# Performance work log

Measured on AMD Instinct MI355X. Metric: run time of the kernel, lower is better.

Reference implementation:

```python
import jax, jax.numpy as jnp
import numpy as np

D_MODEL = 1024
NUM_HEADS = 16
DEPTH = D_MODEL // NUM_HEADS
B, S = 2, 2048


def setup_inputs() -> dict:
    key = jax.random.key(0)
    ks = jax.random.split(key, 12)
    s = 1.0 / np.sqrt(D_MODEL)
    return {
        "query": jax.random.normal(ks[0], (B, S, D_MODEL), jnp.float32),
        "key": jax.random.normal(ks[1], (B, S, D_MODEL), jnp.float32),
        "value": jax.random.normal(ks[2], (B, S, D_MODEL), jnp.float32),
        "mask": jax.random.randint(ks[3], (B, S), 0, 2, jnp.int32),
        "Wq": jax.random.normal(ks[4], (D_MODEL, D_MODEL), jnp.float32) * s,
        "bq": jnp.zeros((D_MODEL,), jnp.float32),
        "Wk": jax.random.normal(ks[5], (D_MODEL, D_MODEL), jnp.float32) * s,
        "bk": jnp.zeros((D_MODEL,), jnp.float32),
        "Wv": jax.random.normal(ks[6], (D_MODEL, D_MODEL), jnp.float32) * s,
        "bv": jnp.zeros((D_MODEL,), jnp.float32),
        "Wo": jax.random.normal(ks[7], (D_MODEL, D_MODEL), jnp.float32) * s,
        "bo": jnp.zeros((D_MODEL,), jnp.float32),
    }


def _split_heads(x):
    # [B, S, D] -> [B, H, S, depth]
    b, s, _ = x.shape
    return x.reshape(b, s, NUM_HEADS, DEPTH).transpose(0, 2, 1, 3)


def reference(query, key, value, mask, Wq, bq, Wk, bk, Wv, bv, Wo, bo):
    q = _split_heads(query @ Wq.T + bq)
    k = _split_heads(key @ Wk.T + bk)
    v = _split_heads(value @ Wv.T + bv)
    scale = 1.0 / jnp.sqrt(jnp.float32(DEPTH))
    # [B, H, Sq, Sk]
    logits = jnp.einsum("bhqd,bhkd->bhqk", q, k) * scale
    logits = logits + mask.astype(logits.dtype)[:, None, None, :] * (-1e9)
    attn = jax.nn.softmax(logits, axis=-1)
    out = jnp.einsum("bhqk,bhkd->bhqd", attn, v)
    out = out.transpose(0, 2, 1, 3).reshape(query.shape[0], -1, D_MODEL)
    return out @ Wo.T + bo
```

## Files before the change

kernel.cpp:

```cpp
#include <hip/hip_runtime.h>

typedef _Float16 half8 __attribute__((ext_vector_type(8)));
typedef _Float16 half4 __attribute__((ext_vector_type(4)));
typedef __fp16  fp16x2 __attribute__((ext_vector_type(2)));
typedef float floatx4 __attribute__((ext_vector_type(4)));

#define D_MODEL 1024
#define NHEAD   16
#define DH      64
#define BATCH   2
#define SEQ     2048
#define M_TOT   4096

#define SCALE_L2E 0.18033688011112042f
#define MASK_L2E  (-1.4426950408889634e9f)

#define GLD_LDS16(g, l)                                                          \
  __builtin_amdgcn_global_load_lds(                                              \
      (const __attribute__((address_space(1))) void*)(g),                        \
      (__attribute__((address_space(3))) void*)(l), 16, 0, 0)

__device__ inline half4 pk4(floatx4 v) {
  union { fp16x2 h2[2]; half4 h4; } u;
  u.h2[0] = __builtin_amdgcn_cvt_pkrtz(v[0], v[1]);
  u.h2[1] = __builtin_amdgcn_cvt_pkrtz(v[2], v[3]);
  return u.h4;
}

__global__ __launch_bounds__(256) void cvt_all(const float* __restrict__ q,
                                               const float* __restrict__ k,
                                               const float* __restrict__ v,
                                               const float* __restrict__ wq,
                                               const float* __restrict__ wk,
                                               const float* __restrict__ wv,
                                               const float* __restrict__ wo,
                                               _Float16* __restrict__ Xall,
                                               _Float16* __restrict__ Wall) {
  int bid = blockIdx.x;
  const float* src;
  _Float16* dst;
  if (bid < 6144) {
    int tsr = bid >> 11;
    src = (tsr == 0) ? q : (tsr == 1) ? k : v;
    dst = Xall + (size_t)tsr * 4194304;
    bid &= 2047;
  } else {
    int w = (bid - 6144) >> 9;
    src = (w == 0) ? wq : (w == 1) ? wk : (w == 2) ? wv : wo;
    dst = Wall + (size_t)w * 1048576;
    bid = (bid - 6144) & 511;
  }
  int off = bid * 2048 + threadIdx.x * 8;
  float4 a = *(const float4*)(src + off);
  float4 b = *(const float4*)(src + off + 4);
  half8 h;
  h[0] = (_Float16)a.x; h[1] = (_Float16)a.y; h[2] = (_Float16)a.z; h[3] = (_Float16)a.w;
  h[4] = (_Float16)b.x; h[5] = (_Float16)b.y; h[6] = (_Float16)b.z; h[7] = (_Float16)b.w;
  *(half8*)(dst + off) = h;
}

__global__ __launch_bounds__(256) void gemm_qkv(const _Float16* __restrict__ Xall,
                                                const _Float16* __restrict__ Wall,
                                                const float* __restrict__ bq,
                                                const float* __restrict__ bk,
                                                const float* __restrict__ bv,
                                                _Float16* __restrict__ Obase) {
  __shared__ alignas(16) char smem[32768];
  _Float16 (*As)[64]  = (_Float16(*)[64])smem;
  _Float16 (*Bs)[64]  = (_Float16(*)[64])(smem + 16384);
  _Float16 (*Ts)[136] = (_Float16(*)[136])smem;

  const int z = blockIdx.z;
  const _Float16* X = Xall + (size_t)z * 4194304;
  const _Float16* W = Wall + (size_t)z * 1048576;
  const float* bias = (z == 0) ? bq : (z == 1) ? bk : bv;
  _Float16* out = Obase + (size_t)z * 4194304;

  const int t = threadIdx.x, lane = t & 63, wave = t >> 6;
  const int wr = wave >> 1, wc = wave & 1;
  const int m0 = blockIdx.y * 128, n0 = blockIdx.x * 128;
  const int fr = lane & 15, quad = lane >> 4, rg = quad * 4;
  const int fsw = fr & 7;

  floatx4 acc[4][4];
  for (int i = 0; i < 4; i++)
    for (int j = 0; j < 4; j++) acc[i][j] = (floatx4){0.f, 0.f, 0.f, 0.f};

  const int rl = lane >> 3, pc = lane & 7;
  const int gcol = ((pc ^ rl) * 8);
  const _Float16* gA[4];
  const _Float16* gB[4];
  _Float16* lA[4];
  _Float16* lB[4];
  for (int i = 0; i < 4; i++) {
    int row = wave * 32 + i * 8 + rl;
    gA[i] = X + (size_t)(m0 + row) * 1024 + gcol;
    gB[i] = W + (size_t)(n0 + row) * 1024 + gcol;
    lA[i] = &As[wave * 32 + i * 8][0];
    lB[i] = &Bs[wave * 32 + i * 8][0];
  }

  for (int k0 = 0; k0 < 1024; k0 += 64) {
    for (int i = 0; i < 4; i++) GLD_LDS16(gA[i] + k0, lA[i]);
    for (int i = 0; i < 4; i++) GLD_LDS16(gB[i] + k0, lB[i]);
    __syncthreads();

    for (int kk = 0; kk < 2; kk++) {
      const int csw = (((kk << 2) | quad) ^ fsw) * 8;
      half8 af[4], bw[4];
      for (int i = 0; i < 4; i++) {
        af[i] = *(const half8*)&As[wr * 64 + i * 16 + fr][csw];
        bw[i] = *(const half8*)&Bs[wc * 64 + i * 16 + fr][csw];
      }
      for (int i = 0; i < 4; i++)
        for (int j = 0; j < 4; j++)
          acc[i][j] = __builtin_amdgcn_mfma_f32_16x16x32_f16(af[i], bw[j], acc[i][j], 0, 0, 0);
    }
    __syncthreads();
  }

  if (z != 2) {
    for (int i = 0; i < 4; i++)
      for (int j = 0; j < 4; j++) {
        int n = n0 + wc * 64 + j * 16 + fr;
        float bv2 = bias[n];
        int hh = n >> 6, d = n & 63;
        for (int r = 0; r < 4; r++) {
          int m = m0 + wr * 64 + i * 16 + rg + r;
          int bb = m >> 11, s = m & 2047;
          out[(((size_t)(bb * NHEAD + hh)) * SEQ + s) * DH + d] =
              (_Float16)(acc[i][j][r] + bv2);
        }
      }
  } else {
    const int bb = m0 >> 11, s0 = m0 & 2047;
    for (int p = 0; p < 2; p++) {
      __syncthreads();
      if (wc == p) {
        for (int j = 0; j < 4; j++) {
          float bv2 = bias[n0 + p * 64 + j * 16 + fr];
          for (int i = 0; i < 4; i++)
            for (int r = 0; r < 4; r++)
              Ts[j * 16 + fr][wr * 64 + i * 16 + rg + r] =
                  (_Float16)(acc[i][j][r] + bv2);
        }
      }
      __syncthreads();
      int dd = t >> 2, c4 = (t & 3) * 32;
      int hh = (n0 >> 6) + p;
      _Float16* dst = out + (((size_t)(bb * NHEAD + hh)) * DH + dd) * SEQ + s0;
      for (int u = 0; u < 4; u++)
        *(half8*)(dst + c4 + u * 8) = *(const half8*)&Ts[dd][c4 + u * 8];
    }
  }
}

__global__ __launch_bounds__(256) void gemm_wo(const _Float16* __restrict__ ctx,
                                               const _Float16* __restrict__ W,
                                               const float* __restrict__ bias,
                                               float* __restrict__ out) {
  __shared__ alignas(16) _Float16 As[128][64];
  __shared__ alignas(16) _Float16 Bs[64][64];

  const int t = threadIdx.x, lane = t & 63, wave = t >> 6;
  const int m0 = blockIdx.y * 128, n0 = blockIdx.x * 64;
  const int fr = lane & 15, quad = lane >> 4, rg = quad * 4;
  const int fsw = fr & 7;

  floatx4 acc[2][4];
  for (int i = 0; i < 2; i++)
    for (int j = 0; j < 4; j++) acc[i][j] = (floatx4){0.f, 0.f, 0.f, 0.f};

  const int rl = lane >> 3, pc = lane & 7;
  const int gcol = ((pc ^ rl) * 8);
  const _Float16* gA[4];
  const _Float16* gB[2];
  _Float16* lA[4];
  _Float16* lB[2];
  for (int i = 0; i < 4; i++) {
    int row = wave * 32 + i * 8 + rl;
    gA[i] = ctx + (size_t)(m0 + row) * 1024 + gcol;
    lA[i] = &As[wave * 32 + i * 8][0];
  }
  for (int i = 0; i < 2; i++) {
    int row = wave * 16 + i * 8 + rl;
    gB[i] = W + (size_t)(n0 + row) * 1024 + gcol;
    lB[i] = &Bs[wave * 16 + i * 8][0];
  }

  for (int k0 = 0; k0 < 1024; k0 += 64) {
    for (int i = 0; i < 4; i++) GLD_LDS16(gA[i] + k0, lA[i]);
    for (int i = 0; i < 2; i++) GLD_LDS16(gB[i] + k0, lB[i]);
    __syncthreads();

    for (int kk = 0; kk < 2; kk++) {
      const int csw = (((kk << 2) | quad) ^ fsw) * 8;
      half8 af[2], bw[4];
      for (int i = 0; i < 2; i++)
        af[i] = *(const half8*)&As[wave * 32 + i * 16 + fr][csw];
      for (int j = 0; j < 4; j++)
        bw[j] = *(const half8*)&Bs[j * 16 + fr][csw];
      for (int i = 0; i < 2; i++)
        for (int j = 0; j < 4; j++)
          acc[i][j] = __builtin_amdgcn_mfma_f32_16x16x32_f16(af[i], bw[j], acc[i][j], 0, 0, 0);
    }
    __syncthreads();
  }

  for (int i = 0; i < 2; i++)
    for (int j = 0; j < 4; j++) {
      int n = n0 + j * 16 + fr;
      float bv2 = bias[n];
      for (int r = 0; r < 4; r++) {
        int m = m0 + wave * 32 + i * 16 + rg + r;
        out[(size_t)m * D_MODEL + n] = acc[i][j][r] + bv2;
      }
    }
}

__global__ __launch_bounds__(256) void attn_kernel(const _Float16* __restrict__ Qp,
                                                   const _Float16* __restrict__ Kp,
                                                   const _Float16* __restrict__ VT,
                                                   const int* __restrict__ mask,
                                                   _Float16* __restrict__ ctx) {
  __shared__ alignas(16) _Float16 Ks[128][64];
  __shared__ alignas(16) _Float16 Vt[64][128];
  __shared__ float Msf[128];

  const int b = blockIdx.z, h = blockIdx.y, q0 = blockIdx.x * 128;
  const int t = threadIdx.x, lane = t & 63, wave = t >> 6;
  const int fr = lane & 15, quad = lane >> 4, fc = quad * 8;
  const int fsw = fr & 7;

  const _Float16* Kg  = Kp + (size_t)(b * NHEAD + h) * SEQ * DH;
  const _Float16* VTg = VT + (size_t)(b * NHEAD + h) * DH * SEQ;

  half8 qf[2][2];
  {
    const _Float16* Qgw = Qp + ((size_t)(b * NHEAD + h) * SEQ + q0 + wave * 32) * DH;
    for (int mi = 0; mi < 2; mi++)
      for (int kk = 0; kk < 2; kk++)
        qf[mi][kk] = *(const half8*)(Qgw + (mi * 16 + fr) * DH + kk * 32 + fc);
  }

  float lrow[2] = {0.f, 0.f};
  floatx4 oaccT[4][2];
  for (int dj = 0; dj < 4; dj++)
    for (int mi = 0; mi < 2; mi++) oaccT[dj][mi] = (floatx4){0.f, 0.f, 0.f, 0.f};

  const int skr = t >> 1;
  const int skc = (t & 1) * 4;
  const int svr = t >> 2;
  const int svc = (t & 3) * 4;

  for (int kt = 0; kt < SEQ / 128; kt++) {
    const int k0 = kt * 128;
    {
      const half8* gk = (const half8*)(Kg + (k0 + skr) * 64);
      for (int u = 0; u < 4; u++)
        *(half8*)&Ks[skr][((skc + u) ^ (skr & 7)) * 8] = gk[skc + u];
      const half8* gv = (const half8*)(VTg + (size_t)svr * SEQ + k0);
      for (int u = 0; u < 4; u++)
        *(half8*)&Vt[svr][((svc + u) ^ (svr & 7)) * 8] = gv[svc + u];
      if (t < 128) Msf[t] = (float)mask[b * SEQ + k0 + t] * MASK_L2E;
    }
    __syncthreads();

    floatx4 saT[8][2];
#pragma unroll
    for (int t8 = 0; t8 < 8; t8++) {
      saT[t8][0] = (floatx4){0.f, 0.f, 0.f, 0.f};
      saT[t8][1] = (floatx4){0.f, 0.f, 0.f, 0.f};
      half8 kf0 = *(const half8*)&Ks[t8 * 16 + fr][(quad ^ fsw) * 8];
      half8 kf1 = *(const half8*)&Ks[t8 * 16 + fr][((4 | quad) ^ fsw) * 8];
      saT[t8][0] = __builtin_amdgcn_mfma_f32_16x16x32_f16(kf0, qf[0][0], saT[t8][0], 0, 0, 0);
      saT[t8][1] = __builtin_amdgcn_mfma_f32_16x16x32_f16(kf0, qf[1][0], saT[t8][1], 0, 0, 0);
      saT[t8][0] = __builtin_amdgcn_mfma_f32_16x16x32_f16(kf1, qf[0][1], saT[t8][0], 0, 0, 0);
      saT[t8][1] = __builtin_amdgcn_mfma_f32_16x16x32_f16(kf1, qf[1][1], saT[t8][1], 0, 0, 0);
    }

    floatx4 mk[8];
#pragma unroll
    for (int t8 = 0; t8 < 8; t8++)
      mk[t8] = *(const floatx4*)&Msf[t8 * 16 + quad * 4];

#pragma unroll
    for (int mi = 0; mi < 2; mi++) {
      float rs = 0.f;
#pragma unroll
      for (int t8 = 0; t8 < 8; t8++)
        for (int r = 0; r < 4; r++) {
          float p = exp2f(saT[t8][mi][r] * SCALE_L2E + mk[t8][r]);
          saT[t8][mi][r] = p;
          rs += p;
        }
      lrow[mi] += rs;
    }

#pragma unroll
    for (int t8 = 0; t8 < 8; t8++) {
      half4 pb0 = pk4(saT[t8][0]);
      half4 pb1 = pk4(saT[t8][1]);
      const int ch0 = t8 * 2 + (quad >> 1);
      const int voff = ((ch0 ^ fsw) * 8) + (quad & 1) * 4;
#pragma unroll
      for (int dj = 0; dj < 4; dj++) {
        half4 va = *(const half4*)&Vt[dj * 16 + fr][voff];
        oaccT[dj][0] = __builtin_amdgcn_mfma_f32_16x16x16f16(va, pb0, oaccT[dj][0], 0, 0, 0);
        oaccT[dj][1] = __builtin_amdgcn_mfma_f32_16x16x16f16(va, pb1, oaccT[dj][1], 0, 0, 0);
      }
    }
    __syncthreads();
  }

#pragma unroll
  for (int mi = 0; mi < 2; mi++) {
    float l = lrow[mi];
    l += __shfl_xor(l, 16);
    l += __shfl_xor(l, 32);
    float inv = 1.0f / l;
    int qrow = q0 + wave * 32 + mi * 16 + fr;
    _Float16* o = ctx + ((size_t)b * SEQ + qrow) * D_MODEL + h * DH;
#pragma unroll
    for (int dj = 0; dj < 4; dj++) {
      half4 st;
      for (int r = 0; r < 4; r++) st[r] = (_Float16)(oaccT[dj][mi][r] * inv);
      *(half4*)(o + dj * 16 + quad * 4) = st;
    }
  }
}

extern "C" void kernel_launch(void* const* d_in, const int* in_sizes, int n_in,
                              void* d_out, int out_size, void* d_ws, size_t ws_size,
                              hipStream_t stream) {
  const float* query = (const float*)d_in[0];
  const float* key   = (const float*)d_in[1];
  const float* value = (const float*)d_in[2];
  const int*   mask  = (const int*)d_in[3];
  const float* Wq = (const float*)d_in[4];
  const float* bq = (const float*)d_in[5];
  const float* Wk = (const float*)d_in[6];
  const float* bk = (const float*)d_in[7];
  const float* Wv = (const float*)d_in[8];
  const float* bv = (const float*)d_in[9];
  const float* Wo = (const float*)d_in[10];
  const float* bo = (const float*)d_in[11];

  char* ws = (char*)d_ws;
  _Float16* Xall = (_Float16*)(ws);
  _Float16* Wall = (_Float16*)(ws + (size_t)24 * 1024 * 1024);
  _Float16* Qp   = (_Float16*)(ws + (size_t)32 * 1024 * 1024);
  _Float16* ctx  = (_Float16*)(ws + (size_t)56 * 1024 * 1024);

  _Float16* Kp = Qp + (size_t)4194304;
  _Float16* VT = Qp + (size_t)8388608;

  cvt_all<<<8192, 256, 0, stream>>>(query, key, value, Wq, Wk, Wv, Wo, Xall, Wall);

  gemm_qkv<<<dim3(8, 32, 3), 256, 0, stream>>>(Xall, Wall, bq, bk, bv, Qp);

  attn_kernel<<<dim3(SEQ / 128, NHEAD, BATCH), 256, 0, stream>>>(Qp, Kp, VT, mask, ctx);

  gemm_wo<<<dim3(16, 32), 256, 0, stream>>>(ctx, Wall + (size_t)3 * 1048576, bo, (float*)d_out);
}
```

Before: 256.8 us.

## Split attention over key halves and add a combine kernel

The attention kernel now splits the key sequence into two halves via a third grid dimension. This doubles the number of workgroups so more CUs are busy. Each half writes an unnormalized fp16 partial output and its row sums to workspace. A new combine kernel adds the two partials and normalizes by the summed denominators before the output projection. The cost is an extra launch, extra global memory traffic for the partials, and fp16 storage of unnormalized accumulators.

```diff
diff --git a/kernel.cpp b/kernel.cpp
--- a/kernel.cpp
+++ b/kernel.cpp
@@ -11,6 +11,7 @@
 #define BATCH   2
 #define SEQ     2048
 #define M_TOT   4096
+#define NT      (SEQ / 128)
 
 #define SCALE_L2E 0.18033688011112042f
 #define MASK_L2E  (-1.4426950408889634e9f)
@@ -222,22 +223,24 @@
                                                    const _Float16* __restrict__ Kp,
                                                    const _Float16* __restrict__ VT,
                                                    const int* __restrict__ mask,
-                                                   _Float16* __restrict__ ctx) {
+                                                   _Float16* __restrict__ Opart,
+                                                   float* __restrict__ lpart) {
   __shared__ alignas(16) _Float16 Ks[128][64];
   __shared__ alignas(16) _Float16 Vt[64][128];
   __shared__ float Msf[128];
 
-  const int b = blockIdx.z, h = blockIdx.y, q0 = blockIdx.x * 128;
+  const int hh = blockIdx.y, q0 = blockIdx.x * 128, half = blockIdx.z;
+  const int b = hh >> 4, h = hh & 15;
   const int t = threadIdx.x, lane = t & 63, wave = t >> 6;
   const int fr = lane & 15, quad = lane >> 4, fc = quad * 8;
   const int fsw = fr & 7;
 
-  const _Float16* Kg  = Kp + (size_t)(b * NHEAD + h) * SEQ * DH;
-  const _Float16* VTg = VT + (size_t)(b * NHEAD + h) * DH * SEQ;
+  const _Float16* Kg  = Kp + (size_t)hh * SEQ * DH;
+  const _Float16* VTg = VT + (size_t)hh * DH * SEQ;
 
   half8 qf[2][2];
   {
-    const _Float16* Qgw = Qp + ((size_t)(b * NHEAD + h) * SEQ + q0 + wave * 32) * DH;
+    const _Float16* Qgw = Qp + ((size_t)hh * SEQ + q0 + wave * 32) * DH;
     for (int mi = 0; mi < 2; mi++)
       for (int kk = 0; kk < 2; kk++)
         qf[mi][kk] = *(const half8*)(Qgw + (mi * 16 + fr) * DH + kk * 32 + fc);
@@ -253,7 +256,8 @@
   const int svr = t >> 2;
   const int svc = (t & 3) * 4;
 
-  for (int kt = 0; kt < SEQ / 128; kt++) {
+  const int ktbase = half * (NT / 2);
+  for (int kt = ktbase; kt < ktbase + NT / 2; kt++) {
     const int k0 = kt * 128;
     {
       const half8* gk = (const half8*)(Kg + (k0 + skr) * 64);
@@ -318,16 +322,38 @@
     float l = lrow[mi];
     l += __shfl_xor(l, 16);
     l += __shfl_xor(l, 32);
-    float inv = 1.0f / l;
     int qrow = q0 + wave * 32 + mi * 16 + fr;
-    _Float16* o = ctx + ((size_t)b * SEQ + qrow) * D_MODEL + h * DH;
+    if (quad == 0)
+      lpart[((size_t)half * 32 + hh) * SEQ + qrow] = l;
+    _Float16* o = Opart + (size_t)half * 4194304 +
+                  ((size_t)b * SEQ + qrow) * D_MODEL + h * DH;
 #pragma unroll
     for (int dj = 0; dj < 4; dj++) {
       half4 st;
-      for (int r = 0; r < 4; r++) st[r] = (_Float16)(oaccT[dj][mi][r] * inv);
+      for (int r = 0; r < 4; r++) st[r] = (_Float16)oaccT[dj][mi][r];
       *(half4*)(o + dj * 16 + quad * 4) = st;
     }
   }
+}
+
+__global__ __launch_bounds__(256) void combine(const _Float16* __restrict__ Opart,
+                                               const float* __restrict__ lpart,
+                                               _Float16* __restrict__ ctx) {
+  int g = blockIdx.x * 256 + threadIdx.x;
+  int m = g >> 7;
+  int d0 = (g & 127) * 8;
+  int b = m >> 11, s = m & 2047, h = d0 >> 6;
+  int hh = b * 16 + h;
+  float l0 = lpart[(size_t)hh * SEQ + s];
+  float l1 = lpart[((size_t)32 + hh) * SEQ + s];
+  float inv = 1.0f / (l0 + l1);
+  half8 o0 = *(const half8*)(Opart + (size_t)m * 1024 + d0);
+  half8 o1 = *(const half8*)(Opart + (size_t)4194304 + (size_t)m * 1024 + d0);
+  half8 r;
+#pragma unroll
+  for (int i = 0; i < 8; i++)
+    r[i] = (_Float16)(((float)o0[i] + (float)o1[i]) * inv);
+  *(half8*)(ctx + (size_t)m * 1024 + d0) = r;
 }
 
 extern "C" void kernel_launch(void* const* d_in, const int* in_sizes, int n_in,
@@ -355,11 +381,16 @@
   _Float16* Kp = Qp + (size_t)4194304;
   _Float16* VT = Qp + (size_t)8388608;
 
+  _Float16* Opart = (_Float16*)(ws);
+  float*    lpart = (float*)(ws + (size_t)16 * 1024 * 1024);
+
   cvt_all<<<8192, 256, 0, stream>>>(query, key, value, Wq, Wk, Wv, Wo, Xall, Wall);
 
   gemm_qkv<<<dim3(8, 32, 3), 256, 0, stream>>>(Xall, Wall, bq, bk, bv, Qp);
 
-  attn_kernel<<<dim3(SEQ / 128, NHEAD, BATCH), 256, 0, stream>>>(Qp, Kp, VT, mask, ctx);
+  attn_kernel<<<dim3(SEQ / 128, 32, 2), 256, 0, stream>>>(Qp, Kp, VT, mask, Opart, lpart);
+
+  combine<<<2048, 256, 0, stream>>>(Opart, lpart, ctx);
 
   gemm_wo<<<dim3(16, 32), 256, 0, stream>>>(ctx, Wall + (size_t)3 * 1048576, bo, (float*)d_out);
 }
```

Result: no change. 260.8 us (+1.6%).

## Load K tiles via global_load_lds, repack V layout for wide reads, flatten grid

Applied to the files above, without the earlier changes.

K tiles are now copied straight from global memory into LDS with global_load_lds and the XOR swizzle is applied on the global address, so the data no longer passes through registers. The V tile is stored in LDS with a permuted layout, which lets the PV loop read one half8 per dj and feed two MFMAs from it, halving the LDS read count. The grid is flattened to 1D with head and batch in the low bits, so blocks that run together share K/V less and spread across heads. This adds index arithmetic and relies on the async LDS load being finished at the existing barrier.

```diff
diff --git a/kernel.cpp b/kernel.cpp
--- a/kernel.cpp
+++ b/kernel.cpp
@@ -11,6 +11,7 @@
 #define BATCH   2
 #define SEQ     2048
 #define M_TOT   4096
+#define NT      (SEQ / 128)
 
 #define SCALE_L2E 0.18033688011112042f
 #define MASK_L2E  (-1.4426950408889634e9f)
@@ -227,17 +228,33 @@
   __shared__ alignas(16) _Float16 Vt[64][128];
   __shared__ float Msf[128];
 
-  const int b = blockIdx.z, h = blockIdx.y, q0 = blockIdx.x * 128;
+  const int bid = blockIdx.x;
+  const int hh = bid & 31;
+  const int q0 = (bid >> 5) * 128;
+  const int b = hh >> 4, h = hh & 15;
+
   const int t = threadIdx.x, lane = t & 63, wave = t >> 6;
   const int fr = lane & 15, quad = lane >> 4, fc = quad * 8;
   const int fsw = fr & 7;
 
-  const _Float16* Kg  = Kp + (size_t)(b * NHEAD + h) * SEQ * DH;
-  const _Float16* VTg = VT + (size_t)(b * NHEAD + h) * DH * SEQ;
+  const _Float16* Kg  = Kp + (size_t)hh * SEQ * DH;
+  const _Float16* VTg = VT + (size_t)hh * DH * SEQ;
+
+  const _Float16* kG[4];
+  {
+    const int kr = lane >> 3, kp = lane & 7;
+    for (int i = 0; i < 4; i++) {
+      int krow = wave * 32 + i * 8 + kr;
+      kG[i] = Kg + (size_t)krow * DH + ((kp ^ kr) * 8);
+    }
+  }
+
+  const int svr = t >> 2;
+  const int svc = (t & 3) * 4;
 
   half8 qf[2][2];
   {
-    const _Float16* Qgw = Qp + ((size_t)(b * NHEAD + h) * SEQ + q0 + wave * 32) * DH;
+    const _Float16* Qgw = Qp + ((size_t)hh * SEQ + q0 + wave * 32) * DH;
     for (int mi = 0; mi < 2; mi++)
       for (int kk = 0; kk < 2; kk++)
         qf[mi][kk] = *(const half8*)(Qgw + (mi * 16 + fr) * DH + kk * 32 + fc);
@@ -248,22 +265,28 @@
   for (int dj = 0; dj < 4; dj++)
     for (int mi = 0; mi < 2; mi++) oaccT[dj][mi] = (floatx4){0.f, 0.f, 0.f, 0.f};
 
-  const int skr = t >> 1;
-  const int skc = (t & 1) * 4;
-  const int svr = t >> 2;
-  const int svc = (t & 3) * 4;
-
-  for (int kt = 0; kt < SEQ / 128; kt++) {
+  for (int kt = 0; kt < NT; kt++) {
     const int k0 = kt * 128;
+
+    for (int i = 0; i < 4; i++)
+      GLD_LDS16(kG[i] + (size_t)k0 * DH, &Ks[wave * 32 + i * 8][0]);
+
     {
-      const half8* gk = (const half8*)(Kg + (k0 + skr) * 64);
-      for (int u = 0; u < 4; u++)
-        *(half8*)&Ks[skr][((skc + u) ^ (skr & 7)) * 8] = gk[skc + u];
       const half8* gv = (const half8*)(VTg + (size_t)svr * SEQ + k0);
-      for (int u = 0; u < 4; u++)
-        *(half8*)&Vt[svr][((svc + u) ^ (svr & 7)) * 8] = gv[svc + u];
-      if (t < 128) Msf[t] = (float)mask[b * SEQ + k0 + t] * MASK_L2E;
-    }
+      half8 vb[4];
+      for (int u = 0; u < 4; u++) vb[u] = gv[svc + u];
+      const int rsw = svr & 7;
+      for (int u = 0; u < 4; u++) {
+        const int g = svc + u;
+        const int t8p = g >> 2, par = (g >> 1) & 1, qA = (g & 1) * 2;
+        const int v4lo = t8p * 8 + qA * 2 + par;
+        const int v4hi = v4lo + 2;
+        union { half8 h8; half4 h4[2]; } uv; uv.h8 = vb[u];
+        *(half4*)&Vt[svr][((v4lo >> 1) ^ rsw) * 8 + (v4lo & 1) * 4] = uv.h4[0];
+        *(half4*)&Vt[svr][((v4hi >> 1) ^ rsw) * 8 + (v4hi & 1) * 4] = uv.h4[1];
+      }
+    }
+    if (t < 128) Msf[t] = (float)mask[b * SEQ + k0 + t] * MASK_L2E;
     __syncthreads();
 
     floatx4 saT[8][2];
@@ -298,16 +321,21 @@
     }
 
 #pragma unroll
-    for (int t8 = 0; t8 < 8; t8++) {
-      half4 pb0 = pk4(saT[t8][0]);
-      half4 pb1 = pk4(saT[t8][1]);
-      const int ch0 = t8 * 2 + (quad >> 1);
-      const int voff = ((ch0 ^ fsw) * 8) + (quad & 1) * 4;
+    for (int t8p = 0; t8p < 4; t8p++) {
+      half4 pb0a = pk4(saT[2 * t8p][0]);
+      half4 pb0b = pk4(saT[2 * t8p][1]);
+      half4 pb1a = pk4(saT[2 * t8p + 1][0]);
+      half4 pb1b = pk4(saT[2 * t8p + 1][1]);
+      const int c = t8p * 4 + quad;
 #pragma unroll
       for (int dj = 0; dj < 4; dj++) {
-        half4 va = *(const half4*)&Vt[dj * 16 + fr][voff];
-        oaccT[dj][0] = __builtin_amdgcn_mfma_f32_16x16x16f16(va, pb0, oaccT[dj][0], 0, 0, 0);
-        oaccT[dj][1] = __builtin_amdgcn_mfma_f32_16x16x16f16(va, pb1, oaccT[dj][1], 0, 0, 0);
+        const int d = dj * 16 + fr;
+        union { half8 h8; half4 h4[2]; } uv;
+        uv.h8 = *(const half8*)&Vt[d][(c ^ (d & 7)) * 8];
+        oaccT[dj][0] = __builtin_amdgcn_mfma_f32_16x16x16f16(uv.h4[0], pb0a, oaccT[dj][0], 0, 0, 0);
+        oaccT[dj][1] = __builtin_amdgcn_mfma_f32_16x16x16f16(uv.h4[0], pb0b, oaccT[dj][1], 0, 0, 0);
+        oaccT[dj][0] = __builtin_amdgcn_mfma_f32_16x16x16f16(uv.h4[1], pb1a, oaccT[dj][0], 0, 0, 0);
+        oaccT[dj][1] = __builtin_amdgcn_mfma_f32_16x16x16f16(uv.h4[1], pb1b, oaccT[dj][1], 0, 0, 0);
       }
     }
     __syncthreads();
@@ -359,7 +387,7 @@
 
   gemm_qkv<<<dim3(8, 32, 3), 256, 0, stream>>>(Xall, Wall, bq, bk, bv, Qp);
 
-  attn_kernel<<<dim3(SEQ / 128, NHEAD, BATCH), 256, 0, stream>>>(Qp, Kp, VT, mask, ctx);
+  attn_kernel<<<dim3(512), 256, 0, stream>>>(Qp, Kp, VT, mask, ctx);
 
   gemm_wo<<<dim3(16, 32), 256, 0, stream>>>(ctx, Wall + (size_t)3 * 1048576, bo, (float*)d_out);
 }
```

Result: faster. 250.1 us (-2.6%).
